# Kernel optimization log

Hardware: AMD Instinct MI355X
Metric: run time of the kernel (lower is better)

## Reference

```python
import jax, jax.numpy as jnp
import numpy as np

N_HEADS = 16
EMBED_DIM = 1024
HEAD_DIM = EMBED_DIM // N_HEADS
SEQ_LEN = 2048


def setup_inputs() -> dict:
    key = jax.random.key(0)
    ks = jax.random.split(key, 9)
    s = 1.0 / np.sqrt(EMBED_DIM)
    inp = {
        "x": jax.random.normal(ks[0], (SEQ_LEN, EMBED_DIM), dtype=jnp.float32),
        "Wq": jax.random.uniform(ks[1], (EMBED_DIM, EMBED_DIM), jnp.float32, -s, s),
        "bq": jax.random.uniform(ks[2], (EMBED_DIM,), jnp.float32, -s, s),
        "Wk": jax.random.uniform(ks[3], (EMBED_DIM, EMBED_DIM), jnp.float32, -s, s),
        "bk": jax.random.uniform(ks[4], (EMBED_DIM,), jnp.float32, -s, s),
        "Wv": jax.random.uniform(ks[5], (EMBED_DIM, EMBED_DIM), jnp.float32, -s, s),
        "bv": jax.random.uniform(ks[6], (EMBED_DIM,), jnp.float32, -s, s),
        "Wo": jax.random.uniform(ks[7], (EMBED_DIM, EMBED_DIM), jnp.float32, -s, s),
        "bo": jax.random.uniform(ks[8], (EMBED_DIM,), jnp.float32, -s, s),
    }
    return inp


def reference(x, Wq, bq, Wk, bk, Wv, bv, Wo, bo):
    # Linear layers (torch convention: y = x @ W.T + b)
    Q = x @ Wq.T + bq  # [S, E]
    K = x @ Wk.T + bk
    V = x @ Wv.T + bv
    # split heads -> [H, S, D]
    def split(t):
        return t.reshape(SEQ_LEN, N_HEADS, HEAD_DIM).transpose(1, 0, 2)
    Qh, Kh, Vh = split(Q), split(K), split(V)
    # NOTE: faithful to source, scale is sqrt(embed_dim), not sqrt(head_dim)
    scale = 1.0 / np.sqrt(EMBED_DIM)
    scores = jnp.einsum("hsd,htd->hst", Qh, Kh) * scale  # [H, S, S]
    attn = jax.nn.softmax(scores, axis=-1)
    ctx = jnp.einsum("hst,htd->hsd", attn, Vh)  # [H, S, D]
    ctx = ctx.transpose(1, 0, 2).reshape(SEQ_LEN, EMBED_DIM)
    out = ctx @ Wo.T + bo
    return (out, attn)
```

## Files before the change

### kernel.cpp

```cpp
#include <hip/hip_runtime.h>
#include <hip/hip_bf16.h>
#include <stdint.h>

#define SQL 2048
#define EMB 1024
#define NHD 16
#define HDD 64

typedef __bf16 bf16x8 __attribute__((ext_vector_type(8)));
typedef __bf16 bf16x4 __attribute__((ext_vector_type(4)));
typedef float f32x4 __attribute__((ext_vector_type(4)));
typedef float f32x16 __attribute__((ext_vector_type(16)));

__device__ __forceinline__ f32x4 mfma16(bf16x8 a, bf16x8 b, f32x4 c) {
    return __builtin_amdgcn_mfma_f32_16x16x32_bf16(a, b, c, 0, 0, 0);
}
__device__ __forceinline__ f32x16 mfma32(bf16x8 a, bf16x8 b, f32x16 c) {
    return __builtin_amdgcn_mfma_f32_32x32x16_bf16(a, b, c, 0, 0, 0);
}

__device__ __forceinline__ void gload_lds16(const __bf16* g, __bf16* lds) {
    __builtin_amdgcn_global_load_lds(
        (const __attribute__((address_space(1))) uint32_t*)g,
        (__attribute__((address_space(3))) uint32_t*)lds,
        16, 0, 0);
}

__global__ void cast5_kernel(const float* __restrict__ x, const float* __restrict__ wq,
                             const float* __restrict__ wk, const float* __restrict__ wv,
                             const float* __restrict__ wo, __bf16* __restrict__ out)
{
    int i = blockIdx.x * blockDim.x + threadIdx.x;
    const float* src; int off;
    if      (i < (512 << 10))  { src = x;  off = 0; }
    else if (i < (768 << 10))  { src = wq; off = 512 << 10; }
    else if (i < (1024 << 10)) { src = wk; off = 768 << 10; }
    else if (i < (1280 << 10)) { src = wv; off = 1024 << 10; }
    else                       { src = wo; off = 1280 << 10; }
    float4 v = ((const float4*)src)[i - off];
    bf16x4 o;
    o[0] = (__bf16)v.x; o[1] = (__bf16)v.y; o[2] = (__bf16)v.z; o[3] = (__bf16)v.w;
    ((bf16x4*)out)[i] = o;
}

template<bool OUT_BF16, bool TRZ2>
__global__ __launch_bounds__(256, 3)
void gemm_bt(const __bf16* __restrict__ A,
             const __bf16* __restrict__ B0, const __bf16* __restrict__ B1, const __bf16* __restrict__ B2,
             const float* __restrict__ bias0, const float* __restrict__ bias1, const float* __restrict__ bias2,
             void* __restrict__ out0, void* __restrict__ out1, void* __restrict__ out2,
             float s0, float s1, float s2,
             int M, int N, int K, int nmtiles)
{
    const int b    = blockIdx.x;
    const int xcd  = b & 7;
    const int idx  = b >> 3;
    const int p    = idx / nmtiles;
    const int bm_i = idx - p * nmtiles;
    const int pid  = xcd + 8 * p;
    const int bn   = (pid & 7) * 128;
    const int bm   = bm_i * 64;
    const int z    = pid >> 3;

    const __bf16* B = B0; const float* bias = bias0; void* Cout = out0; float cscale = s0;
    if (z == 1) { B = B1; bias = bias1; Cout = out1; cscale = s1; }
    if (z == 2) { B = B2; bias = bias2; Cout = out2; cscale = s2; }

    __shared__ __attribute__((aligned(16))) __bf16 As[2][64 * 64];
    __shared__ __attribute__((aligned(16))) __bf16 Bs[2][128 * 64];

    const int tid  = threadIdx.x;
    const int lane = tid & 63;
    const int wave = tid >> 6;
    const int lrow = lane & 15;
    const int quad = lane >> 4;
    const int wm = (wave >> 1) * 32;
    const int wn = (wave & 1) * 64;

    const f32x4 fzero = {0.f, 0.f, 0.f, 0.f};
    f32x4 acc[2][4];
#pragma unroll
    for (int i = 0; i < 2; i++)
#pragma unroll
        for (int j = 0; j < 4; j++) acc[i][j] = fzero;

    const int srow  = lane >> 3;
    const int sslot = (lane & 7) ^ srow;

    auto stage = [&](int sbuf, int k0) {
#pragma unroll
        for (int j = 0; j < 2; j++) {
            int r0 = wave * 16 + j * 8;
            gload_lds16(&A[(size_t)(bm + r0 + srow) * K + k0 + sslot * 8], &As[sbuf][r0 * 64]);
        }
#pragma unroll
        for (int j = 0; j < 4; j++) {
            int r0 = wave * 32 + j * 8;
            gload_lds16(&B[(size_t)(bn + r0 + srow) * K + k0 + sslot * 8], &Bs[sbuf][r0 * 64]);
        }
    };

    const int nt = K >> 6;
    int buf = 0;
    stage(0, 0);
    __syncthreads();

    for (int t = 0; t < nt; t++) {
        if (t < nt - 1) stage(buf ^ 1, (t + 1) * 64);
        bf16x8 af[2][2], bfr[4][2];
#pragma unroll
        for (int i = 0; i < 2; i++) {
            int ra = wm + i * 16 + lrow;
#pragma unroll
            for (int ks = 0; ks < 2; ks++) {
                int sa = (((ks << 2) | quad) ^ (ra & 7)) << 3;
                af[i][ks] = *(const bf16x8*)&As[buf][ra * 64 + sa];
            }
        }
#pragma unroll
        for (int i = 0; i < 4; i++) {
            int rb = wn + i * 16 + lrow;
#pragma unroll
            for (int ks = 0; ks < 2; ks++) {
                int sb = (((ks << 2) | quad) ^ (rb & 7)) << 3;
                bfr[i][ks] = *(const bf16x8*)&Bs[buf][rb * 64 + sb];
            }
        }
#pragma unroll
        for (int ks = 0; ks < 2; ks++)
#pragma unroll
            for (int mi = 0; mi < 2; mi++)
#pragma unroll
                for (int ni = 0; ni < 4; ni++)
                    acc[mi][ni] = mfma16(af[mi][ks], bfr[ni][ks], acc[mi][ni]);
        __syncthreads();
        buf ^= 1;
    }

    const bool trz = TRZ2 && (z == 2);
#pragma unroll
    for (int mi = 0; mi < 2; mi++) {
        int row = bm + wm + mi * 16 + quad * 4;
#pragma unroll
        for (int ni = 0; ni < 4; ni++) {
            int col = bn + wn + ni * 16 + lrow;
            float bv = bias[col];
            if (trz) {
                bf16x4 t;
#pragma unroll
                for (int r = 0; r < 4; r++) t[r] = (__bf16)((acc[mi][ni][r] + bv) * cscale);
                *(bf16x4*)&((__bf16*)Cout)[(size_t)col * SQL + row] = t;
            } else {
#pragma unroll
                for (int r = 0; r < 4; r++) {
                    float v = (acc[mi][ni][r] + bv) * cscale;
                    if (OUT_BF16) ((__bf16*)Cout)[(size_t)(row + r) * N + col] = (__bf16)v;
                    else          ((float*)Cout)[(size_t)(row + r) * N + col] = v;
                }
            }
        }
    }
}

__global__ __launch_bounds__(256, 2)
void attn_kernel(const __bf16* __restrict__ Qg, const __bf16* __restrict__ Kg,
                 const __bf16* __restrict__ Vt, float* __restrict__ attn,
                 __bf16* __restrict__ ctx)
{
    __shared__ __attribute__((aligned(16))) __bf16 Ks[2][64 * 64];
    __shared__ __attribute__((aligned(16))) __bf16 Vs[2][64 * 64];
    __shared__ __attribute__((aligned(16))) float  Pf[2][64 * 68];
    __shared__ float Lb[4][64];
    float* Ored = &Pf[0][0];

    const int tid  = threadIdx.x;
    const int lane = tid & 63;
    const int w    = tid >> 6;
    const int wq   = w & 1;
    const int wk   = w >> 1;
    const int l31  = lane & 31;
    const int hi   = lane >> 5;

    const int b    = blockIdx.x;
    const int xcd  = b & 7;
    const int slot = b >> 3;
    const int h    = xcd + ((slot >> 5) << 3);
    const int q0   = (slot & 31) * 64;

    const f32x16 Z16 = {0.f,0.f,0.f,0.f,0.f,0.f,0.f,0.f,0.f,0.f,0.f,0.f,0.f,0.f,0.f,0.f};

    bf16x8 qf[2][4];
#pragma unroll
    for (int qg = 0; qg < 2; qg++) {
        const __bf16* qp = &Qg[(size_t)(q0 + qg * 32 + l31) * EMB + h * HDD + hi * 8];
#pragma unroll
        for (int ds = 0; ds < 4; ds++) qf[qg][ds] = *(const bf16x8*)&qp[ds * 16];
    }

    {
        const __bf16* kp = &Kg[(size_t)(w * 32 + l31) * EMB + h * HDD + hi * 8];
        const size_t tstep = (size_t)128 * EMB;
        bf16x8 kcur[4], knxt[4];
#pragma unroll
        for (int ds = 0; ds < 4; ds++) kcur[ds] = *(const bf16x8*)&kp[ds * 16];
        float ls0 = 0.f, ls1 = 0.f;
        for (int t = 0; t < 16; t++) {
            if (t < 15) {
#pragma unroll
                for (int ds = 0; ds < 4; ds++)
                    knxt[ds] = *(const bf16x8*)&kp[(size_t)(t + 1) * tstep + ds * 16];
            }
            f32x16 sA = Z16, sB = Z16;
            __builtin_amdgcn_s_setprio(1);
#pragma unroll
            for (int ds = 0; ds < 4; ds++) {
                sA = mfma32(kcur[ds], qf[0][ds], sA);
                sB = mfma32(kcur[ds], qf[1][ds], sB);
            }
            __builtin_amdgcn_s_setprio(0);
#pragma unroll
            for (int r = 0; r < 16; r++) { ls0 += __expf(sA[r]); ls1 += __expf(sB[r]); }
            if (t < 15) {
#pragma unroll
                for (int ds = 0; ds < 4; ds++) kcur[ds] = knxt[ds];
            }
        }
        ls0 += __shfl_xor(ls0, 32);
        ls1 += __shfl_xor(ls1, 32);
        if (hi == 0) { Lb[w][l31] = ls0; Lb[w][32 + l31] = ls1; }
    }

    const int srow  = lane >> 3;
    const int sslot = (lane & 7) ^ (srow & 7);
    auto stageK = [&](int buf, int k0) {
#pragma unroll
        for (int j = 0; j < 2; j++) {
            int r = w * 16 + j * 8;
            gload_lds16(&Kg[(size_t)(k0 + r + srow) * EMB + h * HDD + sslot * 8],
                        &Ks[buf][r * 64]);
        }
    };
    auto stageV = [&](int buf, int k0) {
#pragma unroll
        for (int j = 0; j < 2; j++) {
            int r = w * 16 + j * 8;
            gload_lds16(&Vt[(size_t)(h * HDD + r + srow) * SQL + k0 + sslot * 8],
                        &Vs[buf][r * 64]);
        }
    };

    stageK(0, 0);
    stageV(0, 0);
    __syncthreads();

    float rinv;
    {
        int q = wq * 32 + l31;
        rinv = 1.f / (Lb[0][q] + Lb[1][q] + Lb[2][q] + Lb[3][q]);
    }

    f32x16 o0 = Z16, o1 = Z16;
    float* __restrict__ attn_h = attn + (size_t)h * SQL * SQL;
    const int krowoff = (wk * 32 + l31) * 64;
    const int lane7   = lane & 7;
    const int vrow0 = l31 * 64;
    const int vrow1 = (32 + l31) * 64;
    const int pq    = (wq * 32 + l31) * 68;
    const bf16x8* qfp = qf[wq];

    int buf = 0;
    for (int t = 0; t < 32; t++) {
        const int k0 = t * 64;
        if (t < 31) { stageK(buf ^ 1, k0 + 64); stageV(buf ^ 1, k0 + 64); }
        f32x16 s = Z16;
#pragma unroll
        for (int ds = 0; ds < 4; ds++) {
            bf16x8 kf = *(const bf16x8*)&Ks[buf][krowoff + ((((ds << 1) | hi) ^ lane7) << 3)];
            s = mfma32(kf, qfp[ds], s);
        }
#pragma unroll
        for (int g = 0; g < 4; g++) {
            f32x4 pv;
#pragma unroll
            for (int i = 0; i < 4; i++) pv[i] = __expf(s[g * 4 + i]) * rinv;
            *(f32x4*)&Pf[buf][pq + wk * 32 + g * 8 + hi * 4] = pv;
        }
#pragma unroll
        for (int kt = 0; kt < 2; kt++) {
            const float* pp = &Pf[buf][pq + wk * 32 + kt * 16 + hi * 8];
            f32x4 pA = *(const f32x4*)pp;
            f32x4 pB = *(const f32x4*)(pp + 4);
            bf16x8 pf;
#pragma unroll
            for (int i = 0; i < 4; i++) { pf[i] = (__bf16)pA[i]; pf[i + 4] = (__bf16)pB[i]; }
            int vslot = (((wk << 2) | (kt << 1) | hi) ^ lane7) << 3;
            bf16x8 v0 = *(const bf16x8*)&Vs[buf][vrow0 + vslot];
            bf16x8 v1 = *(const bf16x8*)&Vs[buf][vrow1 + vslot];
            o0 = mfma32(v0, pf, o0);
            o1 = mfma32(v1, pf, o1);
        }
        __syncthreads();
#pragma unroll
        for (int j = 0; j < 4; j++) {
            int lin = j * 256 + tid;
            int r   = lin >> 4;
            int c   = (lin & 15) << 2;
            f32x4 v = *(const f32x4*)&Pf[buf][r * 68 + c];
            *(f32x4*)&attn_h[(size_t)(q0 + r) * SQL + k0 + c] = v;
        }
        buf ^= 1;
    }

    if (wk == 1) {
#pragma unroll
        for (int g = 0; g < 4; g++)
#pragma unroll
            for (int i = 0; i < 4; i++) {
                int dl = i + g * 8 + hi * 4;
                Ored[dl * 66 + wq * 32 + l31]        = o0[g * 4 + i];
                Ored[(32 + dl) * 66 + wq * 32 + l31] = o1[g * 4 + i];
            }
    }
    __syncthreads();
    if (wk == 0) {
        __bf16* crow = &ctx[(size_t)(q0 + wq * 32 + l31) * EMB + h * HDD];
#pragma unroll
        for (int g = 0; g < 4; g++) {
            bf16x4 c0, c1;
#pragma unroll
            for (int i = 0; i < 4; i++) {
                int dl = i + g * 8 + hi * 4;
                c0[i] = (__bf16)(o0[g * 4 + i] + Ored[dl * 66 + wq * 32 + l31]);
                c1[i] = (__bf16)(o1[g * 4 + i] + Ored[(32 + dl) * 66 + wq * 32 + l31]);
            }
            *(bf16x4*)&crow[g * 8 + hi * 4]      = c0;
            *(bf16x4*)&crow[32 + g * 8 + hi * 4] = c1;
        }
    }
}

extern "C" void kernel_launch(void* const* d_in, const int* in_sizes, int n_in,
                              void* d_out, int out_size, void* d_ws, size_t ws_size,
                              hipStream_t stream)
{
    const float* x  = (const float*)d_in[0];
    const float* Wq = (const float*)d_in[1];
    const float* bq = (const float*)d_in[2];
    const float* Wk = (const float*)d_in[3];
    const float* bk = (const float*)d_in[4];
    const float* Wv = (const float*)d_in[5];
    const float* bv = (const float*)d_in[6];
    const float* Wo = (const float*)d_in[7];
    const float* bo = (const float*)d_in[8];

    float* out  = (float*)d_out;
    float* attn = out + (size_t)SQL * EMB;

    const size_t M1 = 1u << 20;
    __bf16* wsb = (__bf16*)d_ws;
    __bf16* xb  = wsb;
    __bf16* wqb = wsb + 2 * M1;
    __bf16* wkb = wsb + 3 * M1;
    __bf16* wvb = wsb + 4 * M1;
    __bf16* wob = wsb + 5 * M1;
    __bf16* Qb  = wsb + 6 * M1;
    __bf16* Kb  = wsb + 8 * M1;
    __bf16* Vtb = wsb + 12 * M1;
    __bf16* ctb = wsb + 14 * M1;

    cast5_kernel<<<6144, 256, 0, stream>>>(x, Wq, Wk, Wv, Wo, wsb);

    gemm_bt<true, true><<<768, 256, 0, stream>>>(
        xb, wqb, wkb, wvb, bq, bk, bv,
        (void*)Qb, (void*)Kb, (void*)Vtb,
        0.03125f, 1.0f, 1.0f, SQL, EMB, EMB, 32);

    attn_kernel<<<512, 256, 0, stream>>>(Qb, Kb, Vtb, attn, ctb);

    gemm_bt<false, false><<<256, 256, 0, stream>>>(
        ctb, wob, wob, wob, bo, bo, bo,
        (void*)out, (void*)out, (void*)out,
        1.0f, 1.0f, 1.0f, SQL, EMB, EMB, 32);
}
```

Before: 387.8 us.

## Drop LDS staging in attention loop; load K/V to registers, store attn directly

Removes the shared-memory double buffers for K, V and the probability tile in the main attention loop. Each wave now loads its K fragments straight from global memory into registers with one-tile-ahead prefetch, and loads V fragments the same way. It rebuilds the bf16 P operand with cross-half-wave shuffles instead of an LDS round trip, and writes attention probabilities to global memory directly from registers. This removes the per-tile __syncthreads and LDS traffic. The cost is duplicated global loads across waves and smaller, strided 32-byte attn stores in place of the earlier row-contiguous writes.

```diff
diff --git a/kernel.cpp b/kernel.cpp
--- a/kernel.cpp
+++ b/kernel.cpp
@@ -167,16 +167,13 @@
                  const __bf16* __restrict__ Vt, float* __restrict__ attn,
                  __bf16* __restrict__ ctx)
 {
-    __shared__ __attribute__((aligned(16))) __bf16 Ks[2][64 * 64];
-    __shared__ __attribute__((aligned(16))) __bf16 Vs[2][64 * 64];
-    __shared__ __attribute__((aligned(16))) float  Pf[2][64 * 68];
     __shared__ float Lb[4][64];
-    float* Ored = &Pf[0][0];
+    __shared__ float Ored[64][66];
 
     const int tid  = threadIdx.x;
     const int lane = tid & 63;
     const int w    = tid >> 6;
-    const int wq   = w & 1;
+    const int p    = w & 1;
     const int wk   = w >> 1;
     const int l31  = lane & 31;
     const int hi   = lane >> 5;
@@ -229,86 +226,86 @@
         ls1 += __shfl_xor(ls1, 32);
         if (hi == 0) { Lb[w][l31] = ls0; Lb[w][32 + l31] = ls1; }
     }
-
-    const int srow  = lane >> 3;
-    const int sslot = (lane & 7) ^ (srow & 7);
-    auto stageK = [&](int buf, int k0) {
-#pragma unroll
-        for (int j = 0; j < 2; j++) {
-            int r = w * 16 + j * 8;
-            gload_lds16(&Kg[(size_t)(k0 + r + srow) * EMB + h * HDD + sslot * 8],
-                        &Ks[buf][r * 64]);
-        }
-    };
-    auto stageV = [&](int buf, int k0) {
-#pragma unroll
-        for (int j = 0; j < 2; j++) {
-            int r = w * 16 + j * 8;
-            gload_lds16(&Vt[(size_t)(h * HDD + r + srow) * SQL + k0 + sslot * 8],
-                        &Vs[buf][r * 64]);
-        }
-    };
-
-    stageK(0, 0);
-    stageV(0, 0);
     __syncthreads();
 
     float rinv;
     {
-        int q = wq * 32 + l31;
+        int q = p * 32 + l31;
         rinv = 1.f / (Lb[0][q] + Lb[1][q] + Lb[2][q] + Lb[3][q]);
     }
 
     f32x16 o0 = Z16, o1 = Z16;
-    float* __restrict__ attn_h = attn + (size_t)h * SQL * SQL;
-    const int krowoff = (wk * 32 + l31) * 64;
-    const int lane7   = lane & 7;
-    const int vrow0 = l31 * 64;
-    const int vrow1 = (32 + l31) * 64;
-    const int pq    = (wq * 32 + l31) * 68;
-    const bf16x8* qfp = qf[wq];
-
-    int buf = 0;
+    float* __restrict__ arow =
+        attn + (size_t)h * SQL * SQL + (size_t)(q0 + p * 32 + l31) * SQL;
+    const __bf16* kp2 = &Kg[(size_t)(wk * 32 + l31) * EMB + h * HDD + hi * 8];
+    const __bf16* vpA = &Vt[(size_t)(h * HDD + l31) * SQL + wk * 32 + hi * 8];
+    const __bf16* vpB = vpA + (size_t)32 * SQL;
+    const bf16x8* qfp = qf[p];
+    const size_t kstep = (size_t)64 * EMB;
+
+    bf16x8 kcur[4], knxt[4];
+#pragma unroll
+    for (int ds = 0; ds < 4; ds++) kcur[ds] = *(const bf16x8*)&kp2[ds * 16];
+
     for (int t = 0; t < 32; t++) {
         const int k0 = t * 64;
-        if (t < 31) { stageK(buf ^ 1, k0 + 64); stageV(buf ^ 1, k0 + 64); }
+        if (t < 31) {
+#pragma unroll
+            for (int ds = 0; ds < 4; ds++)
+                knxt[ds] = *(const bf16x8*)&kp2[(size_t)(t + 1) * kstep + ds * 16];
+        }
+        bf16x8 vA[2], vB[2];
+#pragma unroll
+        for (int kt = 0; kt < 2; kt++) {
+            vA[kt] = *(const bf16x8*)&vpA[k0 + kt * 16];
+            vB[kt] = *(const bf16x8*)&vpB[k0 + kt * 16];
+        }
         f32x16 s = Z16;
-#pragma unroll
-        for (int ds = 0; ds < 4; ds++) {
-            bf16x8 kf = *(const bf16x8*)&Ks[buf][krowoff + ((((ds << 1) | hi) ^ lane7) << 3)];
-            s = mfma32(kf, qfp[ds], s);
-        }
+        __builtin_amdgcn_s_setprio(1);
+#pragma unroll
+        for (int ds = 0; ds < 4; ds++) s = mfma32(kcur[ds], qfp[ds], s);
+        __builtin_amdgcn_s_setprio(0);
+
+        float pv[16];
 #pragma unroll
         for (int g = 0; g < 4; g++) {
-            f32x4 pv;
-#pragma unroll
-            for (int i = 0; i < 4; i++) pv[i] = __expf(s[g * 4 + i]) * rinv;
-            *(f32x4*)&Pf[buf][pq + wk * 32 + g * 8 + hi * 4] = pv;
-        }
+            f32x4 st4;
+#pragma unroll
+            for (int i = 0; i < 4; i++) {
+                float pe = __expf(s[g * 4 + i]) * rinv;
+                pv[g * 4 + i] = pe;
+                st4[i] = pe;
+            }
+            *(f32x4*)&arow[k0 + wk * 32 + g * 8 + hi * 4] = st4;
+        }
+
+        bf16x8 pf[2];
 #pragma unroll
         for (int kt = 0; kt < 2; kt++) {
-            const float* pp = &Pf[buf][pq + wk * 32 + kt * 16 + hi * 8];
-            f32x4 pA = *(const f32x4*)pp;
-            f32x4 pB = *(const f32x4*)(pp + 4);
-            bf16x8 pf;
-#pragma unroll
-            for (int i = 0; i < 4; i++) { pf[i] = (__bf16)pA[i]; pf[i + 4] = (__bf16)pB[i]; }
-            int vslot = (((wk << 2) | (kt << 1) | hi) ^ lane7) << 3;
-            bf16x8 v0 = *(const bf16x8*)&Vs[buf][vrow0 + vslot];
-            bf16x8 v1 = *(const bf16x8*)&Vs[buf][vrow1 + vslot];
-            o0 = mfma32(v0, pf, o0);
-            o1 = mfma32(v1, pf, o1);
-        }
-        __syncthreads();
-#pragma unroll
-        for (int j = 0; j < 4; j++) {
-            int lin = j * 256 + tid;
-            int r   = lin >> 4;
-            int c   = (lin & 15) << 2;
-            f32x4 v = *(const f32x4*)&Pf[buf][r * 68 + c];
-            *(f32x4*)&attn_h[(size_t)(q0 + r) * SQL + k0 + c] = v;
-        }
-        buf ^= 1;
+            float rcv[4];
+#pragma unroll
+            for (int jj = 0; jj < 4; jj++) {
+                float snd = hi ? pv[8 * kt + jj] : pv[8 * kt + 4 + jj];
+                rcv[jj] = __shfl_xor(snd, 32);
+            }
+#pragma unroll
+            for (int j = 0; j < 4; j++) {
+                pf[kt][j]     = (__bf16)(hi ? rcv[j]            : pv[8 * kt + j]);
+                pf[kt][4 + j] = (__bf16)(hi ? pv[8 * kt + 4 + j] : rcv[j]);
+            }
+        }
+
+        __builtin_amdgcn_s_setprio(1);
+        o0 = mfma32(vA[0], pf[0], o0);
+        o0 = mfma32(vA[1], pf[1], o0);
+        o1 = mfma32(vB[0], pf[0], o1);
+        o1 = mfma32(vB[1], pf[1], o1);
+        __builtin_amdgcn_s_setprio(0);
+
+        if (t < 31) {
+#pragma unroll
+            for (int ds = 0; ds < 4; ds++) kcur[ds] = knxt[ds];
+        }
     }
 
     if (wk == 1) {
@@ -317,21 +314,21 @@
 #pragma unroll
             for (int i = 0; i < 4; i++) {
                 int dl = i + g * 8 + hi * 4;
-                Ored[dl * 66 + wq * 32 + l31]        = o0[g * 4 + i];
-                Ored[(32 + dl) * 66 + wq * 32 + l31] = o1[g * 4 + i];
+                Ored[dl][p * 32 + l31]      = o0[g * 4 + i];
+                Ored[32 + dl][p * 32 + l31] = o1[g * 4 + i];
             }
     }
     __syncthreads();
     if (wk == 0) {
-        __bf16* crow = &ctx[(size_t)(q0 + wq * 32 + l31) * EMB + h * HDD];
+        __bf16* crow = &ctx[(size_t)(q0 + p * 32 + l31) * EMB + h * HDD];
 #pragma unroll
         for (int g = 0; g < 4; g++) {
             bf16x4 c0, c1;
 #pragma unroll
             for (int i = 0; i < 4; i++) {
                 int dl = i + g * 8 + hi * 4;
-                c0[i] = (__bf16)(o0[g * 4 + i] + Ored[dl * 66 + wq * 32 + l31]);
-                c1[i] = (__bf16)(o1[g * 4 + i] + Ored[(32 + dl) * 66 + wq * 32 + l31]);
+                c0[i] = (__bf16)(o0[g * 4 + i] + Ored[dl][p * 32 + l31]);
+                c1[i] = (__bf16)(o1[g * 4 + i] + Ored[32 + dl][p * 32 + l31]);
             }
             *(bf16x4*)&crow[g * 8 + hi * 4]      = c0;
             *(bf16x4*)&crow[32 + g * 8 + hi * 4] = c1;
```

Result: slower. 419.5 us (+8.2%).
